# Optimization experiments

Measured on AMD Instinct MI355X. Metric: run time of the kernel, lower is better.

The kernel has to match this reference:

```python
import jax, jax.numpy as jnp
import numpy as np

N_WIRES = 8
DIM = 2 ** N_WIRES  # 256


def _rx(theta):
    # theta: [] or [N] -> [2,2] or [N,2,2] complex64
    c = jnp.cos(theta / 2)
    s = jnp.sin(theta / 2)
    return jnp.stack([jnp.stack([c + 0j, -1j * s], -1),
                      jnp.stack([-1j * s, c + 0j], -1)], -2)


def _ry(theta):
    c = jnp.cos(theta / 2)
    s = jnp.sin(theta / 2)
    return jnp.stack([jnp.stack([c + 0j, -s + 0j], -1),
                      jnp.stack([s + 0j, c + 0j], -1)], -2)


def _rz(theta):
    e = jnp.exp(-1j * theta / 2)
    z = jnp.zeros_like(e)
    return jnp.stack([jnp.stack([e, z], -1),
                      jnp.stack([z, jnp.conj(e)], -1)], -2)


def _apply_1q(state, U, wire):
    # state: [N, DIM]; U: [2,2] (shared) or [N,2,2] (per-sample)
    s = state.reshape(-1, 2 ** wire, 2, 2 ** (N_WIRES - 1 - wire))
    if U.ndim == 2:
        s = jnp.einsum('ab,nxby->nxay', U, s)
    else:
        s = jnp.einsum('nab,nxby->nxay', U, s)
    return s.reshape(-1, DIM)


def _cnot(state, c, t):
    # wire 0 = most significant bit (PennyLane convention)
    s = state.reshape((-1,) + (2,) * N_WIRES)
    ax_c = 1 + c
    s0 = jnp.take(s, 0, axis=ax_c)
    s1 = jnp.take(s, 1, axis=ax_c)
    ax_t = 1 + t if t < c else t  # target axis after control axis removed
    s1 = jnp.flip(s1, axis=ax_t)
    s = jnp.stack([s0, s1], axis=ax_c)
    return s.reshape(-1, DIM)


def _z_signs():
    idx = np.arange(DIM)
    bits = (idx[:, None] >> (N_WIRES - 1 - np.arange(N_WIRES))[None, :]) & 1
    return jnp.asarray(1.0 - 2.0 * bits, dtype=jnp.float32)  # [DIM, 8]


def _circuit(x_flat, params):
    # x_flat: [N, 8] angles; params: [8, 3]
    n = x_flat.shape[0]
    state = jnp.zeros((n, DIM), dtype=jnp.complex64).at[:, 0].set(1.0)
    for i in range(N_WIRES):
        state = _apply_1q(state, _rx(x_flat[:, i]), i)
    for i in range(N_WIRES):
        state = _apply_1q(state, _ry(params[i, 0]), i)
        state = _apply_1q(state, _rz(params[i, 1]), i)
        state = _apply_1q(state, _rx(params[i, 2]), i)
    for i in range(N_WIRES - 1):
        state = _cnot(state, i, i + 1)
    state = _cnot(state, N_WIRES - 1, 0)
    probs = state.real ** 2 + state.imag ** 2  # [N, DIM]
    return probs @ _z_signs()  # [N, 8] PauliZ expvals


def setup_inputs() -> dict:
    key = jax.random.key(0)
    ks = jax.random.split(key, 4)
    B, S = 16, 2048
    embed_dim, ffn_dim = 512, 2048
    return {
        'x': jax.random.normal(ks[0], (B, S, N_WIRES), dtype=jnp.float32),
        'params': jax.random.normal(ks[1], (N_WIRES, 3), dtype=jnp.float32),
        'W1': jax.random.normal(ks[2], (ffn_dim, N_WIRES), dtype=jnp.float32) * 0.1,
        'b1': jnp.zeros((ffn_dim,), dtype=jnp.float32),
        'W2': jax.random.normal(ks[3], (embed_dim, ffn_dim), dtype=jnp.float32) * 0.02,
        'b2': jnp.zeros((embed_dim,), dtype=jnp.float32),
    }


def reference(x, params, W1, b1, W2, b2):
    B, S, _ = x.shape
    ev = _circuit(x.reshape(-1, N_WIRES), params).reshape(B, S, N_WIRES)
    h = jax.nn.relu(ev @ W1.T + b1)
    return h @ W2.T + b2
```

## Files before the change

kernel.cpp:

```cpp
#include <hip/hip_runtime.h>
#include <hip/hip_bf16.h>

#define NS 32768
#define EMB 512
#define KDIM 2048
#define BM 256
#define BN 128
#define NITER (KDIM / 32)

typedef float f32x16 __attribute__((ext_vector_type(16)));
typedef __bf16 bf16x8 __attribute__((ext_vector_type(8)));
typedef __bf16 bf16x2 __attribute__((ext_vector_type(2)));
typedef unsigned int u32;
typedef unsigned int u32x2 __attribute__((ext_vector_type(2)));
typedef const __attribute__((address_space(1))) u32* gptr_t;
typedef __attribute__((address_space(3))) u32* lptr_t;

#if __has_builtin(__builtin_amdgcn_permlane32_swap)
#define HAS_PLS 1
#else
#define HAS_PLS 0
#endif

__device__ __forceinline__ void gload_lds16(const void* g, void* l) {
    __builtin_amdgcn_global_load_lds((gptr_t)g, (lptr_t)l, 16, 0, 0);
}

__device__ __forceinline__ u32 pkrelu(float lo, float hi) {
    union { bf16x2 h; u32 u; } c;
    c.h[0] = (__bf16)fmaxf(lo, 0.f);
    c.h[1] = (__bf16)fmaxf(hi, 0.f);
    return c.u;
}

__device__ __forceinline__ bf16x8 mk_af(u32 a, u32 b, u32 c, u32 d) {
    union { u32 u[4]; bf16x8 v; } t;
    t.u[0] = a; t.u[1] = b; t.u[2] = c; t.u[3] = d;
    return t.v;
}

__device__ __forceinline__ void h_to_af(const f32x16 h, int lane, int half,
                                        bf16x8& af0, bf16x8& af1) {
    u32 w0  = pkrelu(h[0],  h[1]);  u32 w1v = pkrelu(h[2],  h[3]);
    u32 wA  = pkrelu(h[4],  h[5]);  u32 wB  = pkrelu(h[6],  h[7]);
    u32 w2v = pkrelu(h[8],  h[9]);  u32 w3v = pkrelu(h[10], h[11]);
    u32 wC  = pkrelu(h[12], h[13]); u32 wD  = pkrelu(h[14], h[15]);
#if HAS_PLS
    { u32x2 r = __builtin_amdgcn_permlane32_swap(w0,  wA, false, false); w0  = r[0]; wA = r[1]; }
    { u32x2 r = __builtin_amdgcn_permlane32_swap(w1v, wB, false, false); w1v = r[0]; wB = r[1]; }
    { u32x2 r = __builtin_amdgcn_permlane32_swap(w2v, wC, false, false); w2v = r[0]; wC = r[1]; }
    { u32x2 r = __builtin_amdgcn_permlane32_swap(w3v, wD, false, false); w3v = r[0]; wD = r[1]; }
    af0 = mk_af(w0, w1v, wA, wB);
    af1 = mk_af(w2v, w3v, wC, wD);
#else
    int pl = lane ^ 32;
    u32 pw0 = __shfl((int)w0,  pl), pw1 = __shfl((int)w1v, pl);
    u32 pwA = __shfl((int)wA,  pl), pwB = __shfl((int)wB,  pl);
    u32 pw2 = __shfl((int)w2v, pl), pw3 = __shfl((int)w3v, pl);
    u32 pwC = __shfl((int)wC,  pl), pwD = __shfl((int)wD,  pl);
    af0 = half ? mk_af(pwA, pwB, wA, wB) : mk_af(w0,  w1v, pw0, pw1);
    af1 = half ? mk_af(pwC, pwD, wC, wD) : mk_af(w2v, w3v, pw2, pw3);
#endif
}

__global__ __launch_bounds__(256) void k_prep(const float* __restrict__ W2,
                                              const float* __restrict__ W1,
                                              __hip_bfloat16* __restrict__ W2b,
                                              __hip_bfloat16* __restrict__ W1bg) {
    int t = threadIdx.x;
    if (blockIdx.x < 1024) {
        int i = (blockIdx.x * 256 + t) * 4;
        float4 v = *(const float4*)(W2 + i);
        __hip_bfloat16 o[4];
        o[0] = __float2bfloat16(v.x); o[1] = __float2bfloat16(v.y);
        o[2] = __float2bfloat16(v.z); o[3] = __float2bfloat16(v.w);
        *(ulong1*)(W2b + i) = *(ulong1*)o;
    } else {
        int j = (blockIdx.x - 1024) * 1024 + t * 4;
        float4 w = *(const float4*)(W1 + j);
        __hip_bfloat16 p[4];
        p[0] = __float2bfloat16(w.x); p[1] = __float2bfloat16(w.y);
        p[2] = __float2bfloat16(w.z); p[3] = __float2bfloat16(w.w);
        *(ulong1*)(W1bg + j) = *(ulong1*)p;
    }
}

__global__ __launch_bounds__(256, 2) void k_gemm(
        const float* __restrict__ x,
        const float* __restrict__ params,
        const __hip_bfloat16* __restrict__ W1bg,
        const float* __restrict__ b1,
        const __hip_bfloat16* __restrict__ W2b,
        const float* __restrict__ b2,
        float* __restrict__ C) {
    __shared__ __hip_bfloat16 Bs[2][8 * 512];
    __shared__ __hip_bfloat16 W1s[KDIM * 8];
    __shared__ float b1s[KDIM];
    __shared__ __hip_bfloat16 evs[BM * 8];

    int tid = threadIdx.x, wave = tid >> 6, lane = tid & 63;
    int l31 = lane & 31, half = lane >> 5;
    int bx = blockIdx.x, bm = bx >> 2, bn = bx & 3;

    {
        float K1[8], K2[8];
        #pragma unroll
        for (int i = 0; i < 8; i++) {
            float a = params[i*3+0], b = params[i*3+1], g = params[i*3+2];
            float sa, ca, sb, cb, sg, cg;
            __sincosf(a, &sa, &ca);
            __sincosf(b, &sb, &cb);
            __sincosf(g, &sg, &cg);
            K1[i] = sa*sb*sg + ca*cg;
            K2[i] = cb*sg;
        }
        int n = bm * BM + tid;
        float4 x0 = *(const float4*)(x + (size_t)n*8);
        float4 x1 = *(const float4*)(x + (size_t)n*8 + 4);
        float xs[8] = {x0.x, x0.y, x0.z, x0.w, x1.x, x1.y, x1.z, x1.w};
        float z[8];
        #pragma unroll
        for (int i = 0; i < 8; i++) {
            float s, c;
            __sincosf(xs[i], &s, &c);
            z[i] = c * K1[i] - s * K2[i];
        }
        float evv[8];
        float p = z[0];
        #pragma unroll
        for (int j = 1; j < 8; j++) { p *= z[j]; evv[j] = p; }
        float sfx = z[7];
        #pragma unroll
        for (int j = 6; j >= 1; j--) sfx *= z[j];
        evv[0] = sfx;
        __hip_bfloat16 o[8];
        #pragma unroll
        for (int i = 0; i < 8; i++) o[i] = __float2bfloat16(evv[i]);
        *(bf16x8*)&evs[tid * 8] = *(bf16x8*)o;
    }
    for (int i = tid; i < KDIM; i += 256) {
        *(bf16x8*)&W1s[i * 8] = *(const bf16x8*)(W1bg + (size_t)i * 8);
        b1s[i] = b1[i];
    }

    const __hip_bfloat16* gBp[2];
    #pragma unroll
    for (int i = 0; i < 2; i++) {
        int f = wave * 2 + i, ni = f >> 1, t = f & 1;
        gBp[i] = W2b + (size_t)(bn*BN + ni*32 + l31) * KDIM + t*16 + half*8;
    }
    #pragma unroll
    for (int i = 0; i < 2; i++) {
        gload_lds16(gBp[i], &Bs[0][(wave*2 + i) * 512]);
        gBp[i] += 32;
    }

    __syncthreads();

    bf16x8 evB0 = *(bf16x8*)&evs[(wave * 64 +      l31) * 8];
    bf16x8 evB1 = *(bf16x8*)&evs[(wave * 64 + 32 + l31) * 8];

    f32x16 acc[8] = {};

    for (int it = 0; it < NITER; ++it) {
        const int k0 = it * 32;
        const int cb = it & 1;

        if (it + 1 < NITER) {
            #pragma unroll
            for (int i = 0; i < 2; i++) {
                gload_lds16(gBp[i], &Bs[cb ^ 1][(wave*2 + i) * 512]);
                gBp[i] += 32;
            }
        }

        bf16x8 w1f = {};
        if (half == 0) w1f = *(const bf16x8*)&W1s[(k0 + l31) * 8];
        float4 c0 = *(const float4*)&b1s[k0 + 4*half];
        float4 c1 = *(const float4*)&b1s[k0 + 8 + 4*half];
        float4 c2 = *(const float4*)&b1s[k0 + 16 + 4*half];
        float4 c3 = *(const float4*)&b1s[k0 + 24 + 4*half];
        f32x16 hb;
        hb[0] = c0.x; hb[1] = c0.y; hb[2]  = c0.z; hb[3]  = c0.w;
        hb[4] = c1.x; hb[5] = c1.y; hb[6]  = c1.z; hb[7]  = c1.w;
        hb[8] = c2.x; hb[9] = c2.y; hb[10] = c2.z; hb[11] = c2.w;
        hb[12] = c3.x; hb[13] = c3.y; hb[14] = c3.z; hb[15] = c3.w;

        f32x16 h0 = __builtin_amdgcn_mfma_f32_32x32x16_bf16(w1f, evB0, hb, 0, 0, 0);
        bf16x8 af00, af01;
        h_to_af(h0, lane, half, af00, af01);
        f32x16 h1 = __builtin_amdgcn_mfma_f32_32x32x16_bf16(w1f, evB1, hb, 0, 0, 0);
        bf16x8 af10, af11;
        h_to_af(h1, lane, half, af10, af11);

        #pragma unroll
        for (int ni = 0; ni < 4; ni++) {
            bf16x8 bfr = *(bf16x8*)&Bs[cb][(ni*2 + 0) * 512 + lane * 8];
            acc[ni]     = __builtin_amdgcn_mfma_f32_32x32x16_bf16(af00, bfr, acc[ni],     0, 0, 0);
            acc[4 + ni] = __builtin_amdgcn_mfma_f32_32x32x16_bf16(af10, bfr, acc[4 + ni], 0, 0, 0);
        }
        #pragma unroll
        for (int ni = 0; ni < 4; ni++) {
            bf16x8 bfr = *(bf16x8*)&Bs[cb][(ni*2 + 1) * 512 + lane * 8];
            acc[ni]     = __builtin_amdgcn_mfma_f32_32x32x16_bf16(af01, bfr, acc[ni],     0, 0, 0);
            acc[4 + ni] = __builtin_amdgcn_mfma_f32_32x32x16_bf16(af11, bfr, acc[4 + ni], 0, 0, 0);
        }

        __syncthreads();
    }

    #pragma unroll
    for (int rg = 0; rg < 2; rg++) {
        int rbase = bm*BM + wave*64 + rg*32 + 4*half;
        #pragma unroll
        for (int ni = 0; ni < 4; ni++) {
            int col = bn*BN + ni*32 + l31;
            float bias = b2[col];
            #pragma unroll
            for (int r = 0; r < 16; r++) {
                int row = rbase + (r & 3) + 8 * (r >> 2);
                C[(size_t)row * EMB + col] = acc[rg*4 + ni][r] + bias;
            }
        }
    }
}

extern "C" void kernel_launch(void* const* d_in, const int* in_sizes, int n_in,
                              void* d_out, int out_size, void* d_ws, size_t ws_size,
                              hipStream_t stream) {
    const float* x      = (const float*)d_in[0];
    const float* params = (const float*)d_in[1];
    const float* W1     = (const float*)d_in[2];
    const float* b1     = (const float*)d_in[3];
    const float* W2     = (const float*)d_in[4];
    const float* b2     = (const float*)d_in[5];
    float* out = (float*)d_out;

    char* ws = (char*)d_ws;
    __hip_bfloat16* W2b  = (__hip_bfloat16*)ws;
    __hip_bfloat16* W1bg = (__hip_bfloat16*)(ws + 2097152);

    k_prep<<<1040, 256, 0, stream>>>(W2, W1, W2b, W1bg);
    k_gemm<<<(NS/BM) * (EMB/BN), 256, 0, stream>>>(x, params, W1bg, b1, W2b, b2, out);
}
```

Measured before the change: 151.8 us.

## Software-pipeline first GEMM one step ahead and fold bias into MFMA

Unrolls the K loop by two and computes the next step's hidden activations (W1·ev MFMA plus ReLU conversion) before issuing the current step's W2 MFMAs, so the dependent first-stage MFMA latency overlaps the second GEMM. The b1 bias is stored as bf16 in LDS and folded into the MFMA through a constant-1 column in the upper half-lane K slot. This replaces four float4 LDS reads per step. s_setprio is raised around the main MFMA block. In exchange it adds register pressure for double A fragments and rounds b1 to bf16.

```diff
diff --git a/kernel.cpp b/kernel.cpp
--- a/kernel.cpp
+++ b/kernel.cpp
@@ -95,7 +95,7 @@
         float* __restrict__ C) {
     __shared__ __hip_bfloat16 Bs[2][8 * 512];
     __shared__ __hip_bfloat16 W1s[KDIM * 8];
-    __shared__ float b1s[KDIM];
+    __shared__ __hip_bfloat16 b1h[KDIM];
     __shared__ __hip_bfloat16 evs[BM * 8];
 
     int tid = threadIdx.x, wave = tid >> 6, lane = tid & 63;
@@ -140,7 +140,7 @@
     }
     for (int i = tid; i < KDIM; i += 256) {
         *(bf16x8*)&W1s[i * 8] = *(const bf16x8*)(W1bg + (size_t)i * 8);
-        b1s[i] = b1[i];
+        b1h[i] = __float2bfloat16(b1[i]);
     }
 
     const __hip_bfloat16* gBp[2];
@@ -157,57 +157,74 @@
 
     __syncthreads();
 
-    bf16x8 evB0 = *(bf16x8*)&evs[(wave * 64 +      l31) * 8];
-    bf16x8 evB1 = *(bf16x8*)&evs[(wave * 64 + 32 + l31) * 8];
+    bf16x8 evB0, evB1;
+    if (half == 0) {
+        evB0 = *(bf16x8*)&evs[(wave * 64 +      l31) * 8];
+        evB1 = *(bf16x8*)&evs[(wave * 64 + 32 + l31) * 8];
+    } else {
+        evB0 = (bf16x8){};
+        evB0[0] = (__bf16)1.0f;
+        evB1 = evB0;
+    }
+    const f32x16 z16 = {};
 
     f32x16 acc[8] = {};
 
-    for (int it = 0; it < NITER; ++it) {
-        const int k0 = it * 32;
-        const int cb = it & 1;
-
-        if (it + 1 < NITER) {
+#define COMPUTE_AF(K0, A00, A01, A10, A11) do {                               \
+        bf16x8 w1f;                                                           \
+        if (half == 0) {                                                      \
+            w1f = *(const bf16x8*)&W1s[((K0) + l31) * 8];                     \
+        } else {                                                              \
+            w1f = (bf16x8){};                                                 \
+            w1f[0] = *(const __bf16*)&b1h[(K0) + l31];                        \
+        }                                                                     \
+        f32x16 h0 = __builtin_amdgcn_mfma_f32_32x32x16_bf16(w1f, evB0, z16, 0, 0, 0); \
+        h_to_af(h0, lane, half, A00, A01);                                    \
+        f32x16 h1 = __builtin_amdgcn_mfma_f32_32x32x16_bf16(w1f, evB1, z16, 0, 0, 0); \
+        h_to_af(h1, lane, half, A10, A11);                                    \
+    } while (0)
+
+#define GEMM2_STEP(CB, A00, A01, A10, A11) do {                               \
+        __builtin_amdgcn_s_setprio(1);                                        \
+        _Pragma("unroll")                                                     \
+        for (int ni = 0; ni < 4; ni++) {                                      \
+            bf16x8 bf0 = *(bf16x8*)&Bs[CB][(ni*2 + 0) * 512 + lane * 8];      \
+            acc[ni]     = __builtin_amdgcn_mfma_f32_32x32x16_bf16(A00, bf0, acc[ni],     0, 0, 0); \
+            acc[4 + ni] = __builtin_amdgcn_mfma_f32_32x32x16_bf16(A10, bf0, acc[4 + ni], 0, 0, 0); \
+            bf16x8 bf1 = *(bf16x8*)&Bs[CB][(ni*2 + 1) * 512 + lane * 8];      \
+            acc[ni]     = __builtin_amdgcn_mfma_f32_32x32x16_bf16(A01, bf1, acc[ni],     0, 0, 0); \
+            acc[4 + ni] = __builtin_amdgcn_mfma_f32_32x32x16_bf16(A11, bf1, acc[4 + ni], 0, 0, 0); \
+        }                                                                     \
+        __builtin_amdgcn_s_setprio(0);                                        \
+    } while (0)
+
+    bf16x8 aA00, aA01, aA10, aA11;
+    bf16x8 aB00, aB01, aB10, aB11;
+    COMPUTE_AF(0, aA00, aA01, aA10, aA11);
+
+    for (int it = 0; it < NITER; it += 2) {
+        #pragma unroll
+        for (int i = 0; i < 2; i++) {
+            gload_lds16(gBp[i], &Bs[1][(wave*2 + i) * 512]);
+            gBp[i] += 32;
+        }
+        COMPUTE_AF((it + 1) * 32, aB00, aB01, aB10, aB11);
+        GEMM2_STEP(0, aA00, aA01, aA10, aA11);
+        __syncthreads();
+
+        if (it + 2 < NITER) {
             #pragma unroll
             for (int i = 0; i < 2; i++) {
-                gload_lds16(gBp[i], &Bs[cb ^ 1][(wave*2 + i) * 512]);
+                gload_lds16(gBp[i], &Bs[0][(wave*2 + i) * 512]);
                 gBp[i] += 32;
             }
-        }
-
-        bf16x8 w1f = {};
-        if (half == 0) w1f = *(const bf16x8*)&W1s[(k0 + l31) * 8];
-        float4 c0 = *(const float4*)&b1s[k0 + 4*half];
-        float4 c1 = *(const float4*)&b1s[k0 + 8 + 4*half];
-        float4 c2 = *(const float4*)&b1s[k0 + 16 + 4*half];
-        float4 c3 = *(const float4*)&b1s[k0 + 24 + 4*half];
-        f32x16 hb;
-        hb[0] = c0.x; hb[1] = c0.y; hb[2]  = c0.z; hb[3]  = c0.w;
-        hb[4] = c1.x; hb[5] = c1.y; hb[6]  = c1.z; hb[7]  = c1.w;
-        hb[8] = c2.x; hb[9] = c2.y; hb[10] = c2.z; hb[11] = c2.w;
-        hb[12] = c3.x; hb[13] = c3.y; hb[14] = c3.z; hb[15] = c3.w;
-
-        f32x16 h0 = __builtin_amdgcn_mfma_f32_32x32x16_bf16(w1f, evB0, hb, 0, 0, 0);
-        bf16x8 af00, af01;
-        h_to_af(h0, lane, half, af00, af01);
-        f32x16 h1 = __builtin_amdgcn_mfma_f32_32x32x16_bf16(w1f, evB1, hb, 0, 0, 0);
-        bf16x8 af10, af11;
-        h_to_af(h1, lane, half, af10, af11);
-
-        #pragma unroll
-        for (int ni = 0; ni < 4; ni++) {
-            bf16x8 bfr = *(bf16x8*)&Bs[cb][(ni*2 + 0) * 512 + lane * 8];
-            acc[ni]     = __builtin_amdgcn_mfma_f32_32x32x16_bf16(af00, bfr, acc[ni],     0, 0, 0);
-            acc[4 + ni] = __builtin_amdgcn_mfma_f32_32x32x16_bf16(af10, bfr, acc[4 + ni], 0, 0, 0);
-        }
-        #pragma unroll
-        for (int ni = 0; ni < 4; ni++) {
-            bf16x8 bfr = *(bf16x8*)&Bs[cb][(ni*2 + 1) * 512 + lane * 8];
-            acc[ni]     = __builtin_amdgcn_mfma_f32_32x32x16_bf16(af01, bfr, acc[ni],     0, 0, 0);
-            acc[4 + ni] = __builtin_amdgcn_mfma_f32_32x32x16_bf16(af11, bfr, acc[4 + ni], 0, 0, 0);
-        }
-
+            COMPUTE_AF((it + 2) * 32, aA00, aA01, aA10, aA11);
+        }
+        GEMM2_STEP(1, aB00, aB01, aB10, aB11);
         __syncthreads();
     }
+#undef COMPUTE_AF
+#undef GEMM2_STEP
 
     #pragma unroll
     for (int rg = 0; rg < 2; rg++) {
```

Result: no change. 151.0 us (-0.6%).
